# Performance work log

Hardware: AMD Instinct MI355X
Metric: run time of the kernel (lower is better)

Reference implementation:

```python
import jax, jax.numpy as jnp
import numpy as np

B, T, T2, C, H = 8, 1024, 257, 1024, 16
D = C // H          # head dim = 64
HID = 256           # global adapter hidden_size
SCALE = 1.0 / np.sqrt(D).astype(np.float32)


def _ln(x, g, b, eps=1e-5):
    mu = jnp.mean(x, -1, keepdims=True)
    var = jnp.mean(jnp.square(x - mu), -1, keepdims=True)
    return (x - mu) * jax.lax.rsqrt(var + eps) * g + b


def setup_inputs() -> dict:
    key = jax.random.key(0)
    ks = jax.random.split(key, 32)
    w = lambda k, shape: jax.random.normal(k, shape, jnp.float32) * 0.02
    inp = {
        'x': jax.random.normal(ks[0], (B, T, C), jnp.float32),
        'enc_x': jax.random.normal(ks[1], (B, T2, C), jnp.float32),
        'ln1_g': jnp.ones((C,), jnp.float32), 'ln1_b': jnp.zeros((C,), jnp.float32),
        'ln2_g': jnp.ones((C,), jnp.float32), 'ln2_b': jnp.zeros((C,), jnp.float32),
        'ln3_g': jnp.ones((C,), jnp.float32), 'ln3_b': jnp.zeros((C,), jnp.float32),
        'attn_qkv_w': w(ks[2], (C, 3 * C)), 'attn_qkv_b': jnp.zeros((3 * C,), jnp.float32),
        'attn_proj_w': w(ks[3], (C, C)), 'attn_proj_b': jnp.zeros((C,), jnp.float32),
        'ca_q_w': w(ks[4], (C, C)), 'ca_q_b': jnp.zeros((C,), jnp.float32),
        'ca_k_w': w(ks[5], (C, C)), 'ca_k_b': jnp.zeros((C,), jnp.float32),
        'ca_v_w': w(ks[6], (C, C)), 'ca_v_b': jnp.zeros((C,), jnp.float32),
        'ca_proj_w': w(ks[7], (C, C)), 'ca_proj_b': jnp.zeros((C,), jnp.float32),
        'fc_w': w(ks[8], (C, 4 * C)), 'fc_b': jnp.zeros((4 * C,), jnp.float32),
        'mlp_proj_w': w(ks[9], (4 * C, C)), 'mlp_proj_b': jnp.zeros((C,), jnp.float32),
        'ad_down_w': w(ks[10], (C, HID)), 'ad_down_b': jnp.zeros((HID,), jnp.float32),
        'ad_up_w': w(ks[11], (HID, C)), 'ad_up_b': jnp.zeros((C,), jnp.float32),
    }
    return inp


def _heads(t, n_tok):  # [B, n_tok, C] -> [B, H, n_tok, D]
    return t.reshape(B, n_tok, H, D).transpose(0, 2, 1, 3)


def _block(x, enc_x, ln1_g, ln1_b, ln2_g, ln2_b, ln3_g, ln3_b,
           attn_qkv_w, attn_qkv_b, attn_proj_w, attn_proj_b,
           ca_q_w, ca_q_b, ca_k_w, ca_k_b, ca_v_w, ca_v_b, ca_proj_w, ca_proj_b,
           fc_w, fc_b, mlp_proj_w, mlp_proj_b,
           ad_down_w, ad_down_b, ad_up_w, ad_up_b):
    # --- causal self-attention ---
    h = _ln(x, ln1_g, ln1_b)
    qkv = h @ attn_qkv_w + attn_qkv_b
    q, k, v = jnp.split(qkv, 3, axis=-1)
    q, k, v = _heads(q, T), _heads(k, T), _heads(v, T)
    att = jnp.einsum('bhtd,bhsd->bhts', q, k) * SCALE
    causal = jnp.tril(jnp.ones((T, T), bool))
    att = jax.nn.softmax(jnp.where(causal, att, -jnp.inf), axis=-1)
    o = jnp.einsum('bhts,bhsd->bthd', att, v).reshape(B, T, C)
    x = x + o @ attn_proj_w + attn_proj_b
    # --- cross-attention (no mask) ---
    h = _ln(x, ln3_g, ln3_b)
    q = _heads(h @ ca_q_w + ca_q_b, T)
    k = _heads(enc_x @ ca_k_w + ca_k_b, T2)
    v = _heads(enc_x @ ca_v_w + ca_v_b, T2)
    att = jax.nn.softmax(jnp.einsum('bhtd,bhsd->bhts', q, k) * SCALE, axis=-1)
    o = jnp.einsum('bhts,bhsd->bthd', att, v).reshape(B, T, C)
    x = x + o @ ca_proj_w + ca_proj_b
    # --- MLP ---
    h = _ln(x, ln2_g, ln2_b)
    x = x + jax.nn.gelu(h @ fc_w + fc_b, approximate=True) @ mlp_proj_w + mlp_proj_b
    # --- adapter (residual inside) ---
    a = jax.nn.relu(x @ ad_down_w + ad_down_b) @ ad_up_w + ad_up_b
    return a + x


def reference(x, enc_x, ln1_g, ln1_b, ln2_g, ln2_b, ln3_g, ln3_b,
              attn_qkv_w, attn_qkv_b, attn_proj_w, attn_proj_b,
              ca_q_w, ca_q_b, ca_k_w, ca_k_b, ca_v_w, ca_v_b, ca_proj_w, ca_proj_b,
              fc_w, fc_b, mlp_proj_w, mlp_proj_b,
              ad_down_w, ad_down_b, ad_up_w, ad_up_b):
    out = _block(x, enc_x, ln1_g, ln1_b, ln2_g, ln2_b, ln3_g, ln3_b,
                 attn_qkv_w, attn_qkv_b, attn_proj_w, attn_proj_b,
                 ca_q_w, ca_q_b, ca_k_w, ca_k_b, ca_v_w, ca_v_b, ca_proj_w, ca_proj_b,
                 fc_w, fc_b, mlp_proj_w, mlp_proj_b,
                 ad_down_w, ad_down_b, ad_up_w, ad_up_b)
    return (out, enc_x)
```

## Files before the change

kernel.cpp:

```cpp
#include <hip/hip_runtime.h>

typedef unsigned short UST;
typedef __attribute__((ext_vector_type(8))) short short8;
typedef __attribute__((ext_vector_type(4))) float f32x4;
typedef __attribute__((ext_vector_type(4))) unsigned short us4;

#define DEV __device__ __forceinline__

DEV float b2f(UST u){ union{unsigned int i; float f;} x; x.i=((unsigned int)u)<<16; return x.f; }
DEV UST f2b(float f){ union{float f; unsigned int i;} x; x.f=f; return (UST)((x.i + 0x7FFFu + ((x.i>>16)&1u))>>16); }
DEV float ldf(const void* p, size_t i, int fl){ return fl ? b2f(((const UST*)p)[i]) : ((const float*)p)[i]; }

DEV void g2l16(const UST* g, UST* l){
  __builtin_amdgcn_global_load_lds((const __attribute__((address_space(1))) unsigned int*)g,
                                   (__attribute__((address_space(3))) unsigned int*)l, 16, 0, 0);
}

__global__ __launch_bounds__(256) void detect_k(const unsigned int* __restrict__ x, int* __restrict__ flag)
{
  int tid = threadIdx.x;
  int cnt = 0;
#pragma unroll
  for (int j=0;j<4;j++){
    unsigned e = (x[tid*4+j] >> 7) & 0xFF;
    cnt += (e >= 100 && e <= 140) ? 1 : 0;
  }
  __shared__ int tot;
  if (tid==0) tot = 0;
  __syncthreads();
  atomicAdd(&tot, cnt);
  __syncthreads();
  if (tid==0) flag[0] = (tot > 512) ? 1 : 0;
}

template<int EPI, bool MTAIL>
__global__ __launch_bounds__(256) void gemm128(
    const UST* __restrict__ A, const UST* __restrict__ Bt, const void* __restrict__ bias,
    int M, int N, int K,
    UST* __restrict__ out, float* __restrict__ resid, void* __restrict__ aux,
    const int* __restrict__ flag)
{
  __shared__ UST As[128*32];
  __shared__ UST Bs[128*32];
  const int fl = flag[0];
  int tid = threadIdx.x;
  int bx = blockIdx.x, by = blockIdx.y;
  int lane = tid & 63, w = tid >> 6;
  int wr = w >> 1, wc = w & 1;
  int lr = lane & 15, lk = (lane >> 4) << 3;

  int c0 = tid, c1 = tid + 256;
  int ar0 = by*128 + (c0>>2), ar1 = by*128 + (c1>>2);
  if (MTAIL){ ar0 = ar0 < M ? ar0 : M-1; ar1 = ar1 < M ? ar1 : M-1; }
  int br0 = bx*128 + (c0>>2), br1 = bx*128 + (c1>>2);
  int ak0 = (c0&3)<<3, ak1 = (c1&3)<<3;
  const UST* pa0 = A + (size_t)ar0*K + ak0;
  const UST* pa1 = A + (size_t)ar1*K + ak1;
  const UST* pb0 = Bt + (size_t)br0*K + ak0;
  const UST* pb1 = Bt + (size_t)br1*K + ak1;
  UST* la0 = &As[c0*8]; UST* la1 = &As[c1*8];
  UST* lb0 = &Bs[c0*8]; UST* lb1 = &Bs[c1*8];

  f32x4 acc[4][4] = {};

  for (int k0 = 0; k0 < K; k0 += 32){
    g2l16(pa0, la0); g2l16(pa1, la1);
    g2l16(pb0, lb0); g2l16(pb1, lb1);
    pa0 += 32; pa1 += 32; pb0 += 32; pb1 += 32;
    __syncthreads();
    short8 af[4], bf[4];
#pragma unroll
    for (int m=0;m<4;m++) af[m] = *(const short8*)&As[(wr*64 + m*16 + lr)*32 + lk];
#pragma unroll
    for (int n=0;n<4;n++) bf[n] = *(const short8*)&Bs[(wc*64 + n*16 + lr)*32 + lk];
#pragma unroll
    for (int m=0;m<4;m++)
#pragma unroll
      for (int n=0;n<4;n++)
        acc[m][n] = __builtin_amdgcn_mfma_f32_16x16x32_bf16(af[m], bf[n], acc[m][n], 0,0,0);
    __syncthreads();
  }

  float bv[4];
#pragma unroll
  for (int n=0;n<4;n++) bv[n] = ldf(bias, bx*128 + wc*64 + n*16 + lr, fl);
#pragma unroll
  for (int m=0;m<4;m++){
#pragma unroll
    for (int r=0;r<4;r++){
      int gr = by*128 + wr*64 + m*16 + ((lane>>4)<<2) + r;
      if (MTAIL && gr >= M) continue;
#pragma unroll
      for (int n=0;n<4;n++){
        int gc = bx*128 + wc*64 + n*16 + lr;
        float v = acc[m][n][r] + bv[n];
        size_t idx = (size_t)gr*N + gc;
        if (EPI == 0){ out[idx] = f2b(v); }
        else if (EPI == 1){ float e = __expf(-1.5957691216f*(v + 0.044715f*v*v*v)); out[idx] = f2b(v/(1.f+e)); }
        else if (EPI == 2){ out[idx] = f2b(v > 0.f ? v : 0.f); }
        else if (EPI == 3){ resid[idx] += v; }
        else if (EPI == 4){ float x2 = resid[idx] + v; resid[idx] = x2; ((UST*)aux)[idx] = f2b(x2); }
        else { float x2 = resid[idx] + v; if (fl) ((UST*)aux)[idx] = f2b(x2); else ((float*)aux)[idx] = x2; }
      }
    }
  }
}

__global__ __launch_bounds__(256) void ln_k(const float* __restrict__ xf, const void* __restrict__ g,
                                            const void* __restrict__ b, UST* __restrict__ out,
                                            const int* __restrict__ flag)
{
  const int fl = flag[0];
  int row = blockIdx.x, tid = threadIdx.x;
  const float* xr = xf + (size_t)row*1024;
  f32x4 v = *(const f32x4*)&xr[tid*4];
  float s = v[0]+v[1]+v[2]+v[3];
  float ss = v[0]*v[0]+v[1]*v[1]+v[2]*v[2]+v[3]*v[3];
#pragma unroll
  for (int off=32; off>0; off>>=1){ s += __shfl_down(s, off); ss += __shfl_down(ss, off); }
  __shared__ float sm[8];
  int w = tid>>6;
  if ((tid&63)==0){ sm[w] = s; sm[4+w] = ss; }
  __syncthreads();
  s = sm[0]+sm[1]+sm[2]+sm[3];
  ss = sm[4]+sm[5]+sm[6]+sm[7];
  float mu = s*(1.f/1024.f);
  float rs = rsqrtf(ss*(1.f/1024.f) - mu*mu + 1e-5f);
  us4 o;
#pragma unroll
  for (int j=0;j<4;j++){
    int c = tid*4+j;
    o[j] = f2b((v[j]-mu)*rs*ldf(g,c,fl) + ldf(b,c,fl));
  }
  *(us4*)&out[(size_t)row*1024 + tid*4] = o;
}

#define NEGBIG (-1e30f)
template<bool CAUSAL>
__global__ __launch_bounds__(256) void attn_k(
    const UST* __restrict__ Qb, size_t qB, int qT,
    const UST* __restrict__ Kb, size_t kB, int kT,
    const UST* __restrict__ Vt, int vS,
    UST* __restrict__ O, int nk)
{
  int qblk = blockIdx.x, bh = blockIdx.y;
  int b = bh >> 4, h = bh & 15;
  int tid = threadIdx.x, w = tid >> 6, lane = tid & 63;
  int lr = lane & 15, lk = (lane >> 4) << 3;
  int t0 = qblk*64 + w*16;
  const UST* q = Qb + (size_t)b*qB + h*64;
  const UST* kp = Kb + (size_t)b*kB + h*64;
  const UST* vp = Vt + (size_t)bh*64*vS;
  short8 qf0 = *(const short8*)&q[(size_t)(t0+lr)*qT + lk];
  short8 qf1 = *(const short8*)&q[(size_t)(t0+lr)*qT + 32 + lk];
  f32x4 oacc[4] = {};
  float m[4], l[4];
#pragma unroll
  for (int r=0;r<4;r++){ m[r] = NEGBIG; l[r] = 0.f; }
  __shared__ UST plds[4][16][32];
  int nt = CAUSAL ? ((t0+15)>>5)+1 : ((nk+31)>>5);
  int qr0 = t0 + ((lane>>4)<<2);
  for (int kt=0; kt<nt; kt++){
    int s0 = kt*32;
    f32x4 sf[2] = {};
#pragma unroll
    for (int half=0; half<2; half++){
      const UST* kr = &kp[(size_t)(s0 + half*16 + lr)*kT + lk];
      short8 k0 = *(const short8*)kr;
      short8 k1 = *(const short8*)(kr + 32);
      sf[half] = __builtin_amdgcn_mfma_f32_16x16x32_bf16(qf0, k0, sf[half], 0,0,0);
      sf[half] = __builtin_amdgcn_mfma_f32_16x16x32_bf16(qf1, k1, sf[half], 0,0,0);
    }
    bool needMask = (CAUSAL && (s0+31 > t0)) || (s0+31 >= nk);
#pragma unroll
    for (int half=0; half<2; half++)
#pragma unroll
      for (int r=0;r<4;r++){
        float sv = sf[half][r]*0.125f;
        if (needMask){
          int key = s0 + half*16 + lr;
          if ((CAUSAL && key > qr0 + r) || key >= nk) sv = NEGBIG;
        }
        sf[half][r] = sv;
      }
    float mx[4];
#pragma unroll
    for (int r=0;r<4;r++) mx[r] = fmaxf(sf[0][r], sf[1][r]);
#pragma unroll
    for (int off=1; off<16; off<<=1)
#pragma unroll
      for (int r=0;r<4;r++) mx[r] = fmaxf(mx[r], __shfl_xor(mx[r], off));
    float scl[4];
#pragma unroll
    for (int r=0;r<4;r++){
      float mn = fmaxf(m[r], mx[r]);
      scl[r] = __expf(m[r] - mn);
      m[r] = mn;
    }
#pragma unroll
    for (int half=0; half<2; half++)
#pragma unroll
      for (int r=0;r<4;r++){
        float d = sf[half][r] - m[r];
        sf[half][r] = (d < -80.f) ? 0.f : __expf(d);
      }
    float sum[4];
#pragma unroll
    for (int r=0;r<4;r++) sum[r] = sf[0][r] + sf[1][r];
#pragma unroll
    for (int off=1; off<16; off<<=1)
#pragma unroll
      for (int r=0;r<4;r++) sum[r] += __shfl_xor(sum[r], off);
#pragma unroll
    for (int r=0;r<4;r++) l[r] = l[r]*scl[r] + sum[r];
#pragma unroll
    for (int nf=0;nf<4;nf++)
#pragma unroll
      for (int r=0;r<4;r++) oacc[nf][r] *= scl[r];
#pragma unroll
    for (int half=0; half<2; half++)
#pragma unroll
      for (int r=0;r<4;r++)
        plds[w][((lane>>4)<<2)+r][half*16+lr] = f2b(sf[half][r]);
    short8 pf = *(const short8*)&plds[w][lr][lk];
#pragma unroll
    for (int nf=0;nf<4;nf++){
      short8 vf = *(const short8*)&vp[(size_t)(nf*16+lr)*vS + s0 + lk];
      oacc[nf] = __builtin_amdgcn_mfma_f32_16x16x32_bf16(pf, vf, oacc[nf], 0,0,0);
    }
  }
#pragma unroll
  for (int nf=0;nf<4;nf++)
#pragma unroll
    for (int r=0;r<4;r++){
      int t = t0 + ((lane>>4)<<2) + r;
      O[(size_t)(b*1024 + t)*1024 + h*64 + nf*16 + lr] = f2b(oacc[nf][r] / l[r]);
    }
}

__global__ __launch_bounds__(256) void transposeW(const void* __restrict__ in, UST* __restrict__ out,
                                                  int K, int N, const int* __restrict__ flag)
{
  const int fl = flag[0];
  int n0 = blockIdx.x*64, k0 = blockIdx.y*64;
  __shared__ UST t[64][72];
  int tid = threadIdx.x;
  int r = tid>>3, cc = (tid&7)*8;
#pragma unroll
  for (int it=0; it<2; it++){
    int k = r + it*32;
    short8 v;
    if (fl){
      v = *(const short8*)&((const UST*)in)[(size_t)(k0+k)*N + n0 + cc];
    } else {
      const float* inf = (const float*)in;
      f32x4 a = *(const f32x4*)&inf[(size_t)(k0+k)*N + n0 + cc];
      f32x4 b = *(const f32x4*)&inf[(size_t)(k0+k)*N + n0 + cc + 4];
#pragma unroll
      for (int j=0;j<4;j++){ v[j] = (short)f2b(a[j]); v[4+j] = (short)f2b(b[j]); }
    }
    *(short8*)&t[k][cc] = v;
  }
  __syncthreads();
#pragma unroll
  for (int it=0; it<2; it++){
    int n = r + it*32;
    short8 v;
#pragma unroll
    for (int j=0;j<8;j++) v[j] = t[cc+j][n];
    *(short8*)&out[(size_t)(n0+n)*K + k0 + cc] = v;
  }
}

__global__ __launch_bounds__(256) void transposeVself(const UST* __restrict__ qkv, UST* __restrict__ vt)
{
  int t0 = blockIdx.x*64; int bh = blockIdx.y; int b = bh>>4, h = bh&15;
  __shared__ UST t[64][72];
  int tid = threadIdx.x, r = tid>>3, cc = (tid&7)*8;
#pragma unroll
  for (int it=0; it<2; it++){
    int tt = r + it*32;
    short8 v = *(const short8*)&qkv[((size_t)(b*1024 + t0 + tt))*3072 + 2048 + h*64 + cc];
    *(short8*)&t[tt][cc] = v;
  }
  __syncthreads();
#pragma unroll
  for (int it=0; it<2; it++){
    int d = r + it*32;
    short8 v;
#pragma unroll
    for (int j=0;j<8;j++) v[j] = t[cc+j][d];
    *(short8*)&vt[((size_t)(bh*64 + d))*1024 + t0 + cc] = v;
  }
}

__global__ __launch_bounds__(256) void transposeVcross(const UST* __restrict__ v2, UST* __restrict__ vt2)
{
  int s0 = blockIdx.x*64; int bh = blockIdx.y; int b = bh>>4, h = bh&15;
  __shared__ UST t[64][72];
  int tid = threadIdx.x, r = tid>>3, cc = (tid&7)*8;
#pragma unroll
  for (int it=0; it<2; it++){
    int s = s0 + r + it*32; if (s > 256) s = 256;
    short8 v = *(const short8*)&v2[((size_t)(b*257 + s))*1024 + h*64 + cc];
    *(short8*)&t[r+it*32][cc] = v;
  }
  __syncthreads();
#pragma unroll
  for (int it=0; it<2; it++){
    int d = r + it*32;
#pragma unroll
    for (int j=0;j<8;j++){
      int s = s0 + cc + j;
      if (s < 257) vt2[((size_t)(bh*64 + d))*288 + s] = t[cc+j][d];
    }
  }
}

__global__ __launch_bounds__(256) void cvt_f32(const void* __restrict__ in, float* __restrict__ out,
                                               const int* __restrict__ flag)
{
  const int fl = flag[0];
  size_t i = ((size_t)blockIdx.x*256 + threadIdx.x)*4;
  f32x4 o;
  if (fl){
    us4 v = *(const us4*)&((const UST*)in)[i];
#pragma unroll
    for (int j=0;j<4;j++) o[j] = b2f(v[j]);
  } else {
    o = *(const f32x4*)&((const float*)in)[i];
  }
  *(f32x4*)&out[i] = o;
}

__global__ __launch_bounds__(256) void encpass(const void* __restrict__ in, UST* __restrict__ enc_c,
                                               void* __restrict__ outp, const int* __restrict__ flag)
{
  const int fl = flag[0];
  size_t i = ((size_t)blockIdx.x*256 + threadIdx.x)*4;
  if (fl){
    us4 v = *(const us4*)&((const UST*)in)[i];
    *(us4*)&enc_c[i] = v;
    *(us4*)&((UST*)outp)[8388608 + i] = v;
  } else {
    f32x4 v = *(const f32x4*)&((const float*)in)[i];
    us4 c;
#pragma unroll
    for (int j=0;j<4;j++) c[j] = f2b(v[j]);
    *(us4*)&enc_c[i] = c;
    *(f32x4*)&((float*)outp)[8388608 + i] = v;
  }
}

extern "C" void kernel_launch(void* const* d_in, const int* in_sizes, int n_in,
                              void* d_out, int out_size, void* d_ws, size_t ws_size,
                              hipStream_t stream) {
  (void)in_sizes; (void)n_in; (void)out_size; (void)ws_size;
  const void* x       = d_in[0];
  const void* enc     = d_in[1];
  const void* ln1g    = d_in[2];
  const void* ln1b    = d_in[3];
  const void* ln2g    = d_in[4];
  const void* ln2b    = d_in[5];
  const void* ln3g    = d_in[6];
  const void* ln3b    = d_in[7];
  const void* qkvW    = d_in[8];
  const void* qkvB    = d_in[9];
  const void* projW   = d_in[10];
  const void* projB   = d_in[11];
  const void* caqW    = d_in[12];
  const void* caqB    = d_in[13];
  const void* cakW    = d_in[14];
  const void* cakB    = d_in[15];
  const void* cavW    = d_in[16];
  const void* cavB    = d_in[17];
  const void* caprojW = d_in[18];
  const void* caprojB = d_in[19];
  const void* fcW     = d_in[20];
  const void* fcB     = d_in[21];
  const void* mlpW    = d_in[22];
  const void* mlpB    = d_in[23];
  const void* adwW    = d_in[24];
  const void* adwB    = d_in[25];
  const void* aupW    = d_in[26];
  const void* aupB    = d_in[27];

  unsigned char* ws = (unsigned char*)d_ws;
  int*   flag = (int*)ws;
  float* xf   = (float*)(ws + 256);
  UST*   big  = (UST*)(ws + 33554688);
  UST*   h    = (UST*)(ws + 100663552);
  UST*   o    = (UST*)(ws + 117440768);
  UST*   wT   = (UST*)(ws + 134217984);
  UST*   encc = (UST*)(ws + 168820992);
  UST* qkvT    = wT;
  UST* projT   = wT + 3145728;
  UST* caqT    = wT + 4194304;
  UST* cakT    = wT + 5242880;
  UST* cavT    = wT + 6291456;
  UST* caprojT = wT + 7340032;
  UST* fcT     = wT + 8388608;
  UST* mlpT    = wT + 12582912;
  UST* adwT    = wT + 16777216;
  UST* aupT    = wT + 17039360;
  UST* q2  = big;
  UST* k2  = big + 8388608;
  UST* v2  = big + 10493952;
  UST* vtX = big + 25165824;

  detect_k<<<1,256,0,stream>>>((const unsigned int*)x, flag);

  transposeW<<<dim3(48,16),256,0,stream>>>(qkvW,    qkvT,    1024, 3072, flag);
  transposeW<<<dim3(16,16),256,0,stream>>>(projW,   projT,   1024, 1024, flag);
  transposeW<<<dim3(16,16),256,0,stream>>>(caqW,    caqT,    1024, 1024, flag);
  transposeW<<<dim3(16,16),256,0,stream>>>(cakW,    cakT,    1024, 1024, flag);
  transposeW<<<dim3(16,16),256,0,stream>>>(cavW,    cavT,    1024, 1024, flag);
  transposeW<<<dim3(16,16),256,0,stream>>>(caprojW, caprojT, 1024, 1024, flag);
  transposeW<<<dim3(64,16),256,0,stream>>>(fcW,     fcT,     1024, 4096, flag);
  transposeW<<<dim3(16,64),256,0,stream>>>(mlpW,    mlpT,    4096, 1024, flag);
  transposeW<<<dim3(4,16), 256,0,stream>>>(adwW,    adwT,    1024, 256,  flag);
  transposeW<<<dim3(16,4), 256,0,stream>>>(aupW,    aupT,    256,  1024, flag);

  cvt_f32<<<8192,256,0,stream>>>(x, xf, flag);
  encpass<<<2056,256,0,stream>>>(enc, encc, d_out, flag);

  ln_k<<<8192,256,0,stream>>>(xf, ln1g, ln1b, h, flag);
  gemm128<0,false><<<dim3(24,64),256,0,stream>>>(h, qkvT, qkvB, 8192, 3072, 1024, big, nullptr, nullptr, flag);
  transposeVself<<<dim3(16,128),256,0,stream>>>(big, vtX);
  attn_k<true><<<dim3(16,128),256,0,stream>>>(big, (size_t)1024*3072, 3072,
                                              big+1024, (size_t)1024*3072, 3072,
                                              vtX, 1024, o, 1024);
  gemm128<3,false><<<dim3(8,64),256,0,stream>>>(o, projT, projB, 8192, 1024, 1024, nullptr, xf, nullptr, flag);

  ln_k<<<8192,256,0,stream>>>(xf, ln3g, ln3b, h, flag);
  gemm128<0,false><<<dim3(8,64),256,0,stream>>>(h, caqT, caqB, 8192, 1024, 1024, q2, nullptr, nullptr, flag);
  gemm128<0,true ><<<dim3(8,17),256,0,stream>>>(encc, cakT, cakB, 2056, 1024, 1024, k2, nullptr, nullptr, flag);
  gemm128<0,true ><<<dim3(8,17),256,0,stream>>>(encc, cavT, cavB, 2056, 1024, 1024, v2, nullptr, nullptr, flag);
  transposeVcross<<<dim3(5,128),256,0,stream>>>(v2, vtX);
  attn_k<false><<<dim3(16,128),256,0,stream>>>(q2, (size_t)1024*1024, 1024,
                                               k2, (size_t)257*1024, 1024,
                                               vtX, 288, o, 257);
  gemm128<3,false><<<dim3(8,64),256,0,stream>>>(o, caprojT, caprojB, 8192, 1024, 1024, nullptr, xf, nullptr, flag);

  ln_k<<<8192,256,0,stream>>>(xf, ln2g, ln2b, h, flag);
  gemm128<1,false><<<dim3(32,64),256,0,stream>>>(h, fcT, fcB, 8192, 4096, 1024, big, nullptr, nullptr, flag);
  gemm128<4,false><<<dim3(8,64),256,0,stream>>>(big, mlpT, mlpB, 8192, 1024, 4096, nullptr, xf, h, flag);

  gemm128<2,false><<<dim3(2,64),256,0,stream>>>(h, adwT, adwB, 8192, 256, 1024, o, nullptr, nullptr, flag);
  gemm128<5,false><<<dim3(8,64),256,0,stream>>>(o, aupT, aupB, 8192, 1024, 256, nullptr, xf, d_out, flag);
}
```

Before: 1.100 ms.

## Stage attention K/V tiles in LDS with double buffering and causal tile pairing

Rewrites the attention kernel so that each block loads 64-key K and V tiles into swizzled, double-buffered LDS with async global-to-LDS copies. All four waves then share those tiles instead of each wave fetching K/V straight from global memory. For causal self-attention, each block handles two query tiles (15-p and p) to even out the triangular work, and the grid is halved. This cuts redundant global traffic and load imbalance, at the cost of more LDS per block and extra block-wide barriers. In cross-attention, the last tile reads past the padded V stride, but those keys are masked.

```diff
diff --git a/kernel.cpp b/kernel.cpp
--- a/kernel.cpp
+++ b/kernel.cpp
@@ -137,105 +137,171 @@
 
 #define NEGBIG (-1e30f)
 template<bool CAUSAL>
-__global__ __launch_bounds__(256) void attn_k(
+__global__ __launch_bounds__(256) void attn2(
     const UST* __restrict__ Qb, size_t qB, int qT,
     const UST* __restrict__ Kb, size_t kB, int kT,
     const UST* __restrict__ Vt, int vS,
     UST* __restrict__ O, int nk)
 {
-  int qblk = blockIdx.x, bh = blockIdx.y;
+  __shared__ UST Ks[2][4096];
+  __shared__ UST Vs[2][4096];
+  __shared__ UST plds[4][16][72];
+
+  int p = blockIdx.x, bh = blockIdx.y;
   int b = bh >> 4, h = bh & 15;
   int tid = threadIdx.x, w = tid >> 6, lane = tid & 63;
-  int lr = lane & 15, lk = (lane >> 4) << 3;
-  int t0 = qblk*64 + w*16;
-  const UST* q = Qb + (size_t)b*qB + h*64;
+  int lr = lane & 15;
+  const UST* q0 = Qb + (size_t)b*qB + h*64;
   const UST* kp = Kb + (size_t)b*kB + h*64;
   const UST* vp = Vt + (size_t)bh*64*vS;
-  short8 qf0 = *(const short8*)&q[(size_t)(t0+lr)*qT + lk];
-  short8 qf1 = *(const short8*)&q[(size_t)(t0+lr)*qT + 32 + lk];
-  f32x4 oacc[4] = {};
-  float m[4], l[4];
-#pragma unroll
-  for (int r=0;r<4;r++){ m[r] = NEGBIG; l[r] = 0.f; }
-  __shared__ UST plds[4][16][32];
-  int nt = CAUSAL ? ((t0+15)>>5)+1 : ((nk+31)>>5);
-  int qr0 = t0 + ((lane>>4)<<2);
-  for (int kt=0; kt<nt; kt++){
-    int s0 = kt*32;
-    f32x4 sf[2] = {};
-#pragma unroll
-    for (int half=0; half<2; half++){
-      const UST* kr = &kp[(size_t)(s0 + half*16 + lr)*kT + lk];
-      short8 k0 = *(const short8*)kr;
-      short8 k1 = *(const short8*)(kr + 32);
-      sf[half] = __builtin_amdgcn_mfma_f32_16x16x32_bf16(qf0, k0, sf[half], 0,0,0);
-      sf[half] = __builtin_amdgcn_mfma_f32_16x16x32_bf16(qf1, k1, sf[half], 0,0,0);
+  const int skmax = nk - 1;
+
+  auto stageK = [&](int bufi, int s0){
+#pragma unroll
+    for (int it=0; it<2; it++){
+      int c = tid + it*256;
+      int s = c >> 3;
+      int srcb = ((c & 7) << 4) ^ ((s & 7) << 4);
+      int sg = s0 + s; sg = sg <= skmax ? sg : skmax;
+      g2l16(kp + (size_t)sg*kT + (srcb>>1), &Ks[bufi][c*8]);
     }
-    bool needMask = (CAUSAL && (s0+31 > t0)) || (s0+31 >= nk);
-#pragma unroll
-    for (int half=0; half<2; half++)
+  };
+  auto stageV = [&](int bufi, int s0){
+#pragma unroll
+    for (int it=0; it<2; it++){
+      int c = tid + it*256;
+      int d = c >> 3;
+      int srcb = ((c & 7) << 4) ^ ((d & 7) << 4);
+      g2l16(vp + (size_t)d*vS + s0 + (srcb>>1), &Vs[bufi][c*8]);
+    }
+  };
+
+  int qtiles[2]; int nq;
+  if (CAUSAL){ qtiles[0] = 15 - p; qtiles[1] = p; nq = 2; }
+  else       { qtiles[0] = p; nq = 1; }
+
+  for (int qi=0; qi<nq; qi++){
+    int qt = qtiles[qi];
+    int t0 = qt*64 + w*16;
+    int qr0 = t0 + ((lane>>4)<<2);
+    short8 qf0 = *(const short8*)&q0[(size_t)(t0+lr)*qT + ((lane>>4)<<3)];
+    short8 qf1 = *(const short8*)&q0[(size_t)(t0+lr)*qT + 32 + ((lane>>4)<<3)];
+    f32x4 oacc[4] = {};
+    float m[4], l[4];
+#pragma unroll
+    for (int r=0;r<4;r++){ m[r] = NEGBIG; l[r] = 0.f; }
+
+    int nt = CAUSAL ? (qt + 1) : ((nk + 63) >> 6);
+    int cur = 0;
+    stageK(0, 0); stageV(0, 0);
+    __syncthreads();
+
+    for (int t=0; t<nt; t++){
+      int s0 = t*64;
+      int nxt = cur ^ 1;
+      if (t+1 < nt){ stageK(nxt, s0 + 64); stageV(nxt, s0 + 64); }
+
+      f32x4 sf[4];
+      const char* ksb = (const char*)&Ks[cur][0];
+      __builtin_amdgcn_s_setprio(1);
+#pragma unroll
+      for (int hf=0; hf<4; hf++){
+        int r = hf*16 + lr;
+        int sw = (r & 7) << 4;
+        int lo = (lane >> 4) << 4;
+        short8 k0 = *(const short8*)(ksb + r*128 + (lo ^ sw));
+        short8 k1 = *(const short8*)(ksb + r*128 + ((64 + lo) ^ sw));
+        f32x4 s_ = {};
+        s_ = __builtin_amdgcn_mfma_f32_16x16x32_bf16(qf0, k0, s_, 0,0,0);
+        s_ = __builtin_amdgcn_mfma_f32_16x16x32_bf16(qf1, k1, s_, 0,0,0);
+        sf[hf] = s_;
+      }
+      __builtin_amdgcn_s_setprio(0);
+
+      bool needMask = (CAUSAL && (s0+63 > t0)) || (s0+63 >= nk);
+#pragma unroll
+      for (int hf=0; hf<4; hf++)
+#pragma unroll
+        for (int r=0;r<4;r++){
+          float sv = sf[hf][r]*0.125f;
+          if (needMask){
+            int key = s0 + hf*16 + lr;
+            if ((CAUSAL && key > qr0 + r) || key >= nk) sv = NEGBIG;
+          }
+          sf[hf][r] = sv;
+        }
+
+      float mx[4];
+#pragma unroll
+      for (int r=0;r<4;r++) mx[r] = fmaxf(fmaxf(sf[0][r], sf[1][r]), fmaxf(sf[2][r], sf[3][r]));
+#pragma unroll
+      for (int off=1; off<16; off<<=1)
+#pragma unroll
+        for (int r=0;r<4;r++) mx[r] = fmaxf(mx[r], __shfl_xor(mx[r], off));
+      float scl[4];
 #pragma unroll
       for (int r=0;r<4;r++){
-        float sv = sf[half][r]*0.125f;
-        if (needMask){
-          int key = s0 + half*16 + lr;
-          if ((CAUSAL && key > qr0 + r) || key >= nk) sv = NEGBIG;
+        float mn = fmaxf(m[r], mx[r]);
+        scl[r] = __expf(m[r] - mn);
+        m[r] = mn;
+      }
+#pragma unroll
+      for (int hf=0; hf<4; hf++)
+#pragma unroll
+        for (int r=0;r<4;r++){
+          float d = sf[hf][r] - m[r];
+          sf[hf][r] = (d < -80.f) ? 0.f : __expf(d);
         }
-        sf[half][r] = sv;
+      float sum[4];
+#pragma unroll
+      for (int r=0;r<4;r++) sum[r] = (sf[0][r] + sf[1][r]) + (sf[2][r] + sf[3][r]);
+#pragma unroll
+      for (int off=1; off<16; off<<=1)
+#pragma unroll
+        for (int r=0;r<4;r++) sum[r] += __shfl_xor(sum[r], off);
+#pragma unroll
+      for (int r=0;r<4;r++) l[r] = l[r]*scl[r] + sum[r];
+#pragma unroll
+      for (int nf=0;nf<4;nf++)
+#pragma unroll
+        for (int r=0;r<4;r++) oacc[nf][r] *= scl[r];
+
+#pragma unroll
+      for (int hf=0; hf<4; hf++)
+#pragma unroll
+        for (int r=0;r<4;r++)
+          plds[w][((lane>>4)<<2)+r][hf*16+lr] = f2b(sf[hf][r]);
+
+      const char* pb = (const char*)&plds[w][0][0];
+      short8 pf0 = *(const short8*)(pb + lr*144 +      ((lane>>4)<<4));
+      short8 pf1 = *(const short8*)(pb + lr*144 + 64 + ((lane>>4)<<4));
+
+      const char* vsb = (const char*)&Vs[cur][0];
+      __builtin_amdgcn_s_setprio(1);
+#pragma unroll
+      for (int nf=0; nf<4; nf++){
+        int d = nf*16 + lr;
+        int sw = (d & 7) << 4;
+        int lo = (lane >> 4) << 4;
+        short8 vf0 = *(const short8*)(vsb + d*128 + (lo ^ sw));
+        short8 vf1 = *(const short8*)(vsb + d*128 + ((64 + lo) ^ sw));
+        oacc[nf] = __builtin_amdgcn_mfma_f32_16x16x32_bf16(pf0, vf0, oacc[nf], 0,0,0);
+        oacc[nf] = __builtin_amdgcn_mfma_f32_16x16x32_bf16(pf1, vf1, oacc[nf], 0,0,0);
       }
-    float mx[4];
-#pragma unroll
-    for (int r=0;r<4;r++) mx[r] = fmaxf(sf[0][r], sf[1][r]);
-#pragma unroll
-    for (int off=1; off<16; off<<=1)
-#pragma unroll
-      for (int r=0;r<4;r++) mx[r] = fmaxf(mx[r], __shfl_xor(mx[r], off));
-    float scl[4];
-#pragma unroll
-    for (int r=0;r<4;r++){
-      float mn = fmaxf(m[r], mx[r]);
-      scl[r] = __expf(m[r] - mn);
-      m[r] = mn;
+      __builtin_amdgcn_s_setprio(0);
+
+      __syncthreads();
+      cur = nxt;
     }
-#pragma unroll
-    for (int half=0; half<2; half++)
+
+#pragma unroll
+    for (int nf=0;nf<4;nf++)
 #pragma unroll
       for (int r=0;r<4;r++){
-        float d = sf[half][r] - m[r];
-        sf[half][r] = (d < -80.f) ? 0.f : __expf(d);
+        int t = t0 + ((lane>>4)<<2) + r;
+        O[(size_t)(b*1024 + t)*1024 + h*64 + nf*16 + lr] = f2b(oacc[nf][r] / l[r]);
       }
-    float sum[4];
-#pragma unroll
-    for (int r=0;r<4;r++) sum[r] = sf[0][r] + sf[1][r];
-#pragma unroll
-    for (int off=1; off<16; off<<=1)
-#pragma unroll
-      for (int r=0;r<4;r++) sum[r] += __shfl_xor(sum[r], off);
-#pragma unroll
-    for (int r=0;r<4;r++) l[r] = l[r]*scl[r] + sum[r];
-#pragma unroll
-    for (int nf=0;nf<4;nf++)
-#pragma unroll
-      for (int r=0;r<4;r++) oacc[nf][r] *= scl[r];
-#pragma unroll
-    for (int half=0; half<2; half++)
-#pragma unroll
-      for (int r=0;r<4;r++)
-        plds[w][((lane>>4)<<2)+r][half*16+lr] = f2b(sf[half][r]);
-    short8 pf = *(const short8*)&plds[w][lr][lk];
-#pragma unroll
-    for (int nf=0;nf<4;nf++){
-      short8 vf = *(const short8*)&vp[(size_t)(nf*16+lr)*vS + s0 + lk];
-      oacc[nf] = __builtin_amdgcn_mfma_f32_16x16x32_bf16(pf, vf, oacc[nf], 0,0,0);
-    }
-  }
-#pragma unroll
-  for (int nf=0;nf<4;nf++)
-#pragma unroll
-    for (int r=0;r<4;r++){
-      int t = t0 + ((lane>>4)<<2) + r;
-      O[(size_t)(b*1024 + t)*1024 + h*64 + nf*16 + lr] = f2b(oacc[nf][r] / l[r]);
-    }
+  }
 }
 
 __global__ __launch_bounds__(256) void transposeW(const void* __restrict__ in, UST* __restrict__ out,
@@ -427,9 +493,9 @@
   ln_k<<<8192,256,0,stream>>>(xf, ln1g, ln1b, h, flag);
   gemm128<0,false><<<dim3(24,64),256,0,stream>>>(h, qkvT, qkvB, 8192, 3072, 1024, big, nullptr, nullptr, flag);
   transposeVself<<<dim3(16,128),256,0,stream>>>(big, vtX);
-  attn_k<true><<<dim3(16,128),256,0,stream>>>(big, (size_t)1024*3072, 3072,
-                                              big+1024, (size_t)1024*3072, 3072,
-                                              vtX, 1024, o, 1024);
+  attn2<true><<<dim3(8,128),256,0,stream>>>(big, (size_t)1024*3072, 3072,
+                                            big+1024, (size_t)1024*3072, 3072,
+                                            vtX, 1024, o, 1024);
   gemm128<3,false><<<dim3(8,64),256,0,stream>>>(o, projT, projB, 8192, 1024, 1024, nullptr, xf, nullptr, flag);
 
   ln_k<<<8192,256,0,stream>>>(xf, ln3g, ln3b, h, flag);
@@ -437,9 +503,9 @@
   gemm128<0,true ><<<dim3(8,17),256,0,stream>>>(encc, cakT, cakB, 2056, 1024, 1024, k2, nullptr, nullptr, flag);
   gemm128<0,true ><<<dim3(8,17),256,0,stream>>>(encc, cavT, cavB, 2056, 1024, 1024, v2, nullptr, nullptr, flag);
   transposeVcross<<<dim3(5,128),256,0,stream>>>(v2, vtX);
-  attn_k<false><<<dim3(16,128),256,0,stream>>>(q2, (size_t)1024*1024, 1024,
-                                               k2, (size_t)257*1024, 1024,
-                                               vtX, 288, o, 257);
+  attn2<false><<<dim3(16,128),256,0,stream>>>(q2, (size_t)1024*1024, 1024,
+                                              k2, (size_t)257*1024, 1024,
+                                              vtX, 288, o, 257);
   gemm128<3,false><<<dim3(8,64),256,0,stream>>>(o, caprojT, caprojB, 8192, 1024, 1024, nullptr, xf, nullptr, flag);
 
   ln_k<<<8192,256,0,stream>>>(xf, ln2g, ln2b, h, flag);
```

Result: faster. 930.4 us (-15.4%).
